# Kernel tuning notes

Hardware: AMD Instinct MI355X
Metric: run time of the kernel (lower is better)

The kernel has to match this reference:

```python
import jax, jax.numpy as jnp
import numpy as np

B, L, K, D = 32, 1024, 1024, 1024

def setup_inputs() -> dict:
    key = jax.random.key(0)
    k1, k2, k3, k4, k5 = jax.random.split(key, 5)
    query = jax.random.normal(k1, (B, L, D), dtype=jnp.float32)
    context = jax.random.normal(k2, (B, K, D), dtype=jnp.float32)
    mask = jax.random.randint(k3, (B * L, K), 0, 2, dtype=jnp.int32)
    W_in = jax.random.normal(k4, (D, D), dtype=jnp.float32) * (D ** -0.5)
    W_out = jax.random.normal(k5, (D, 2 * D), dtype=jnp.float32) * ((2 * D) ** -0.5)
    return {"query": query, "context": context, "mask": mask, "W_in": W_in, "W_out": W_out}

def reference(query, context, mask, W_in, W_out):
    b, l, d = query.shape
    k = context.shape[1]
    # linear_in (general attention): q @ W_in.T
    q = jnp.einsum('bld,ed->ble', query, W_in)
    # attention scores [b, l, k]
    scores = jnp.einsum('bld,bkd->blk', q, context)
    # multiplicative-mask softmax with renormalization (masked_softmax, non-memory-efficient path)
    m = mask.astype(scores.dtype).reshape(b, l, k)
    w = jax.nn.softmax(scores * m, axis=-1) * m
    w = w / (jnp.sum(w, axis=-1, keepdims=True) + 1e-13)
    # mix attended context, concat with transformed query, project, tanh
    mix = jnp.einsum('blk,bkd->bld', w, context)
    combined = jnp.concatenate([mix, q], axis=-1)          # [b, l, 2d]
    out = jnp.tanh(jnp.einsum('blc,dc->bld', combined, W_out))
    return out
```

## Files before the change

### kernel.cpp

```cpp
#include <hip/hip_runtime.h>
#include <math.h>

typedef __bf16 bf16_t;
typedef __bf16 bf16x4 __attribute__((ext_vector_type(4)));
typedef __bf16 bf16x8 __attribute__((ext_vector_type(8)));
typedef _Float16 f16x4 __attribute__((ext_vector_type(4)));
typedef _Float16 f16x8 __attribute__((ext_vector_type(8)));
typedef float f32x4 __attribute__((ext_vector_type(4)));

#define MFMA_BF16 __builtin_amdgcn_mfma_f32_16x16x32_bf16
#define MFMA_F16  __builtin_amdgcn_mfma_f32_16x16x32_f16


__device__ __forceinline__ bf16_t to_bf16_rne(float x, float& rep) {
    unsigned u = __builtin_bit_cast(unsigned, x);
    unsigned r = u + 0x7fffu + ((u >> 16) & 1u);
    unsigned short h = (unsigned short)(r >> 16);
    rep = __builtin_bit_cast(float, ((unsigned)h) << 16);
    return __builtin_bit_cast(bf16_t, h);
}

__device__ __forceinline__ void g2l16(const void* g, void* l) {
    __builtin_amdgcn_global_load_lds(
        (const __attribute__((address_space(1))) unsigned int*)g,
        (__attribute__((address_space(3))) unsigned int*)l, 16, 0, 0);
}

__device__ __forceinline__ int lch(int r, int j) {
    return (r * 8 + (j ^ (r & 7))) * 8;
}

template <typename T>
__device__ __forceinline__ void stage2(const T* __restrict__ gA, long long ldA,
                                       const T* __restrict__ gB, long long ldB,
                                       T* buf, int tid) {
    int wid = tid >> 6, lane = tid & 63;
#pragma unroll
    for (int i = 0; i < 4; ++i) {
        int cb = i * 512 + wid * 64;
        int c = cb + lane;
        int r = c >> 3, j = (c & 7) ^ (r & 7);
        g2l16(gA + (long long)r * ldA + j * 8, buf + (size_t)cb * 8);
    }
#pragma unroll
    for (int i = 0; i < 4; ++i) {
        int cb = i * 512 + wid * 64;
        int c = cb + lane;
        int r = c >> 3, j = (c & 7) ^ (r & 7);
        g2l16(gB + (long long)r * ldB + j * 8, buf + 16384 + (size_t)cb * 8);
    }
}


__global__ __launch_bounds__(256) void split_int_k(const float* __restrict__ in,
                                                   bf16_t* __restrict__ out,
                                                   long long n4) {
    long long i = (long long)blockIdx.x * 256 + threadIdx.x;
    if (i >= n4) return;
    f32x4 v = ((const f32x4*)in)[i];
    bf16x4 hv, lv;
#pragma unroll
    for (int j = 0; j < 4; ++j) {
        float rep;
        hv[j] = to_bf16_rne(v[j], rep);
        float res = v[j] - rep;
        float rep2;
        lv[j] = to_bf16_rne(res, rep2);
    }
    long long row = i >> 8;
    int k = (int)(i & 255) * 4;
    long long base = row * 2048 + ((k >> 5) << 6) + (k & 31);
    *(bf16x4*)(out + base) = hv;
    *(bf16x4*)(out + base + 32) = lv;
}

__global__ __launch_bounds__(256) void cast_f16_k(const float* __restrict__ in,
                                                  _Float16* __restrict__ o, long long n4) {
    long long i = (long long)blockIdx.x * 256 + threadIdx.x;
    if (i >= n4) return;
    f32x4 v = ((const f32x4*)in)[i];
    f16x4 h;
#pragma unroll
    for (int j = 0; j < 4; ++j) h[j] = (_Float16)v[j];
    ((f16x4*)o)[i] = h;
}

__global__ __launch_bounds__(256) void transpose_ctx_k(const float* __restrict__ ctx,
                                                       _Float16* __restrict__ ctxT) {
    __shared__ _Float16 t[32][34];
    int b = blockIdx.z;
    int k0 = blockIdx.x * 32, d0 = blockIdx.y * 32;
    const float* src = ctx + ((long long)b * 1024 + k0) * 1024 + d0;
#pragma unroll
    for (int i = 0; i < 4; ++i) {
        int y = threadIdx.y + i * 8;
        t[y][threadIdx.x] = (_Float16)src[(long long)y * 1024 + threadIdx.x];
    }
    __syncthreads();
    _Float16* dst = ctxT + ((long long)b * 1024 + d0) * 1024 + k0;
#pragma unroll
    for (int i = 0; i < 4; ++i) {
        int y = threadIdx.y + i * 8;
        dst[(long long)y * 1024 + threadIdx.x] = t[threadIdx.x][y];
    }
}

__global__ __launch_bounds__(256) void masked_softmax_k(const float* __restrict__ s,
                                                        const int* __restrict__ m,
                                                        _Float16* __restrict__ w) {
    long long row = blockIdx.x;
    const float* sr = s + row * 1024;
    const int* mr = m + row * 1024;
    _Float16* wr_ = w + row * 1024;
    int t = threadIdx.x;
    int lane = t & 63, wid = t >> 6;
    float v[4];
    int mk[4];
    float mx = -3.0e38f;
#pragma unroll
    for (int i = 0; i < 4; ++i) {
        int idx = t + i * 256;
        v[i] = sr[idx];
        mk[i] = mr[idx];
        if (mk[i]) mx = fmaxf(mx, v[i]);
    }
#pragma unroll
    for (int off = 32; off; off >>= 1) mx = fmaxf(mx, __shfl_xor(mx, off));
    __shared__ float rm[4], rs[4];
    if (!lane) rm[wid] = mx;
    __syncthreads();
    mx = fmaxf(fmaxf(rm[0], rm[1]), fmaxf(rm[2], rm[3]));
    float sum = 0.f;
#pragma unroll
    for (int i = 0; i < 4; ++i) {
        float e = mk[i] ? expf(v[i] - mx) : 0.f;
        v[i] = e;
        sum += e;
    }
#pragma unroll
    for (int off = 32; off; off >>= 1) sum += __shfl_xor(sum, off);
    if (!lane) rs[wid] = sum;
    __syncthreads();
    sum = rs[0] + rs[1] + rs[2] + rs[3];
    float inv = sum > 0.f ? 1.0f / sum : 0.f;
#pragma unroll
    for (int i = 0; i < 4; ++i) wr_[t + i * 256] = (_Float16)(v[i] * inv);
}

template <int EPI>
__global__ __launch_bounds__(512, 2) void gemm_x3_256(
    const bf16_t* __restrict__ Aint, const bf16_t* __restrict__ Bint,
    long long sA, long long sB, long long sC, int nbx, int nby,
    float* __restrict__ Cs, bf16_t* __restrict__ Qint, _Float16* __restrict__ Qf) {
    __shared__ bf16_t lds[65536];
    const int NT = 32;
    int tid = threadIdx.x, lane = tid & 63, wid = tid >> 6;
    int wr = wid >> 2, wc = wid & 3;
    int nwg = gridDim.x;
    int bid = blockIdx.x;
    int lid = (bid & 7) * (nwg >> 3) + (bid >> 3);
    int by = lid % nby;
    int t2 = lid / nby;
    int bx = t2 % nbx;
    int z = t2 / nbx;
    const bf16_t* At = Aint + (long long)z * sA + (long long)bx * 256 * 2048;
    const bf16_t* Bt = Bint + (long long)z * sB + (long long)by * 256 * 2048;
    stage2(At, 2048ll, Bt, 2048ll, lds, tid);
    stage2(At + 64, 2048ll, Bt + 64, 2048ll, lds + 32768, tid);
    f32x4 acc[8][4] = {};
    for (int t = 0; t < NT; ++t) {
        bf16_t* buf = lds + (size_t)(t & 1) * 32768;
        bf16_t* bufB = buf + 16384;
        if (t < NT - 1) {
            asm volatile("s_waitcnt vmcnt(8)" ::: "memory");
        } else {
            asm volatile("s_waitcnt vmcnt(0)" ::: "memory");
        }
        __builtin_amdgcn_sched_barrier(0);
        __builtin_amdgcn_s_barrier();
        __builtin_amdgcn_sched_barrier(0);
        bf16x8 bh[4], bl[4];
#pragma unroll
        for (int n = 0; n < 4; ++n) {
            int rB = wc * 64 + n * 16 + (lane & 15);
            bh[n] = *(const bf16x8*)(bufB + lch(rB, lane >> 4));
            bl[n] = *(const bf16x8*)(bufB + lch(rB, 4 + (lane >> 4)));
        }
#pragma unroll
        for (int p = 0; p < 3; ++p) {
            bf16x8 ah[2], al[2];
#pragma unroll
            for (int i = 0; i < 2; ++i) {
                int rA = wr * 128 + (p * 2 + i) * 16 + (lane & 15);
                ah[i] = *(const bf16x8*)(buf + lch(rA, lane >> 4));
                al[i] = *(const bf16x8*)(buf + lch(rA, 4 + (lane >> 4)));
            }
            __builtin_amdgcn_s_setprio(1);
#pragma unroll
            for (int i = 0; i < 2; ++i)
#pragma unroll
                for (int n = 0; n < 4; ++n) {
                    f32x4 a = acc[p * 2 + i][n];
                    a = MFMA_BF16(ah[i], bh[n], a, 0, 0, 0);
                    a = MFMA_BF16(ah[i], bl[n], a, 0, 0, 0);
                    a = MFMA_BF16(al[i], bh[n], a, 0, 0, 0);
                    acc[p * 2 + i][n] = a;
                }
            __builtin_amdgcn_s_setprio(0);
        }
        bf16x8 ah3[2], al3[2];
#pragma unroll
        for (int i = 0; i < 2; ++i) {
            int rA = wr * 128 + (6 + i) * 16 + (lane & 15);
            ah3[i] = *(const bf16x8*)(buf + lch(rA, lane >> 4));
            al3[i] = *(const bf16x8*)(buf + lch(rA, 4 + (lane >> 4)));
        }
        asm volatile("s_waitcnt lgkmcnt(0)" ::: "memory");
        __builtin_amdgcn_sched_barrier(0);
        __builtin_amdgcn_s_barrier();
        __builtin_amdgcn_sched_barrier(0);
        if (t + 2 < NT)
            stage2(At + (long long)(t + 2) * 64, 2048ll, Bt + (long long)(t + 2) * 64,
                   2048ll, buf, tid);
        __builtin_amdgcn_s_setprio(1);
#pragma unroll
        for (int i = 0; i < 2; ++i)
#pragma unroll
            for (int n = 0; n < 4; ++n) {
                f32x4 a = acc[6 + i][n];
                a = MFMA_BF16(ah3[i], bh[n], a, 0, 0, 0);
                a = MFMA_BF16(ah3[i], bl[n], a, 0, 0, 0);
                a = MFMA_BF16(al3[i], bh[n], a, 0, 0, 0);
                acc[6 + i][n] = a;
            }
        __builtin_amdgcn_s_setprio(0);
    }
    int r0 = bx * 256 + wr * 128 + ((lane >> 4) << 2);
    int c0 = by * 256 + wc * 64 + (lane & 15);
#pragma unroll
    for (int m = 0; m < 8; ++m)
#pragma unroll
        for (int n = 0; n < 4; ++n)
#pragma unroll
            for (int j = 0; j < 4; ++j) {
                int r = r0 + m * 16 + j;
                int c = c0 + n * 16;
                float v = acc[m][n][j];
                if (EPI == 0) {
                    Cs[(long long)z * sC + (long long)r * 1024 + c] = v;
                } else {
                    float rep;
                    bf16_t hb = to_bf16_rne(v, rep);
                    float res = v - rep;
                    float rep2;
                    bf16_t lb = to_bf16_rne(res, rep2);
                    long long rb = (long long)r * 2048 + ((c >> 5) << 6) + (c & 31);
                    Qint[rb] = hb;
                    Qint[rb + 32] = lb;
                    Qf[(long long)r * 1024 + c] = (_Float16)v;
                }
            }
}

template <int EPI>
__global__ __launch_bounds__(512, 2) void gemm_f16_256(
    const _Float16* __restrict__ A1, const _Float16* __restrict__ A2,
    const _Float16* __restrict__ B,
    long long ldA, long long ldB, long long sA, long long sB, long long sC,
    int NT, int swt, int nbx, int nby,
    _Float16* __restrict__ Cm, float* __restrict__ Co) {
    __shared__ _Float16 lds[65536];
    int tid = threadIdx.x, lane = tid & 63, wid = tid >> 6;
    int wr = wid >> 2, wc = wid & 3;
    int nwg = gridDim.x;
    int bid = blockIdx.x;
    int lid = (bid & 7) * (nwg >> 3) + (bid >> 3);
    int by = lid % nby;
    int t2 = lid / nby;
    int bx = t2 % nbx;
    int z = t2 / nbx;
    const _Float16* A1t = A1 + (long long)z * sA + (long long)bx * 256 * ldA;
    const _Float16* A2t = A2 + (long long)bx * 256 * ldA;
    const _Float16* Bt = B + (long long)z * sB + (long long)by * 256 * ldB;
    stage2((0 < swt) ? A1t : A2t, ldA, Bt, ldB, lds, tid);
    stage2((1 < swt) ? A1t + 64 : A2t + (long long)(1 - swt) * 64, ldA, Bt + 64, ldB,
           lds + 32768, tid);
    f32x4 acc[8][4] = {};
    for (int t = 0; t < NT; ++t) {
        _Float16* buf = lds + (size_t)(t & 1) * 32768;
        _Float16* bufB = buf + 16384;
        if (t < NT - 1) {
            asm volatile("s_waitcnt vmcnt(8)" ::: "memory");
        } else {
            asm volatile("s_waitcnt vmcnt(0)" ::: "memory");
        }
        __builtin_amdgcn_sched_barrier(0);
        __builtin_amdgcn_s_barrier();
        __builtin_amdgcn_sched_barrier(0);
        f16x8 bfr[4][2];
#pragma unroll
        for (int n = 0; n < 4; ++n)
#pragma unroll
            for (int ks = 0; ks < 2; ++ks) {
                int rB = wc * 64 + n * 16 + (lane & 15);
                bfr[n][ks] = *(const f16x8*)(bufB + lch(rB, ks * 4 + (lane >> 4)));
            }
#pragma unroll
        for (int p = 0; p < 3; ++p) {
            f16x8 a[2][2];
#pragma unroll
            for (int i = 0; i < 2; ++i)
#pragma unroll
                for (int ks = 0; ks < 2; ++ks) {
                    int rA = wr * 128 + (p * 2 + i) * 16 + (lane & 15);
                    a[i][ks] = *(const f16x8*)(buf + lch(rA, ks * 4 + (lane >> 4)));
                }
            __builtin_amdgcn_s_setprio(1);
#pragma unroll
            for (int i = 0; i < 2; ++i)
#pragma unroll
                for (int n = 0; n < 4; ++n) {
                    f32x4 v = acc[p * 2 + i][n];
                    v = MFMA_F16(a[i][0], bfr[n][0], v, 0, 0, 0);
                    v = MFMA_F16(a[i][1], bfr[n][1], v, 0, 0, 0);
                    acc[p * 2 + i][n] = v;
                }
            __builtin_amdgcn_s_setprio(0);
        }
        f16x8 a3[2][2];
#pragma unroll
        for (int i = 0; i < 2; ++i)
#pragma unroll
            for (int ks = 0; ks < 2; ++ks) {
                int rA = wr * 128 + (6 + i) * 16 + (lane & 15);
                a3[i][ks] = *(const f16x8*)(buf + lch(rA, ks * 4 + (lane >> 4)));
            }
        asm volatile("s_waitcnt lgkmcnt(0)" ::: "memory");
        __builtin_amdgcn_sched_barrier(0);
        __builtin_amdgcn_s_barrier();
        __builtin_amdgcn_sched_barrier(0);
        if (t + 2 < NT) {
            int tt = t + 2;
            const _Float16* gA =
                (tt < swt) ? A1t + (long long)tt * 64 : A2t + (long long)(tt - swt) * 64;
            stage2(gA, ldA, Bt + (long long)tt * 64, ldB, buf, tid);
        }
        __builtin_amdgcn_s_setprio(1);
#pragma unroll
        for (int i = 0; i < 2; ++i)
#pragma unroll
            for (int n = 0; n < 4; ++n) {
                f32x4 v = acc[6 + i][n];
                v = MFMA_F16(a3[i][0], bfr[n][0], v, 0, 0, 0);
                v = MFMA_F16(a3[i][1], bfr[n][1], v, 0, 0, 0);
                acc[6 + i][n] = v;
            }
        __builtin_amdgcn_s_setprio(0);
    }
    int r0 = bx * 256 + wr * 128 + ((lane >> 4) << 2);
    int c0 = by * 256 + wc * 64 + (lane & 15);
#pragma unroll
    for (int m = 0; m < 8; ++m)
#pragma unroll
        for (int n = 0; n < 4; ++n)
#pragma unroll
            for (int j = 0; j < 4; ++j) {
                int r = r0 + m * 16 + j;
                int c = c0 + n * 16;
                float v = acc[m][n][j];
                if (EPI == 0) {
                    Cm[(long long)z * sC + (long long)r * 1024 + c] = (_Float16)v;
                } else {
                    Co[(long long)r * 1024 + c] = tanhf(v);
                }
            }
}


extern "C" void kernel_launch(void* const* d_in, const int* in_sizes, int n_in,
                              void* d_out, int out_size, void* d_ws, size_t ws_size,
                              hipStream_t stream) {
    const float* query = (const float*)d_in[0];
    const float* ctx = (const float*)d_in[1];
    const int* mask = (const int*)d_in[2];
    const float* Win = (const float*)d_in[3];
    const float* Wout = (const float*)d_in[4];
    float* outp = (float*)d_out;

    const long long MB = 1048576ll;
    int G = 1;
    if ((long long)ws_size >= 648 * MB) G = 32;
    else if ((long long)ws_size >= 328 * MB) G = 16;
    else if ((long long)ws_size >= 168 * MB) G = 8;
    else if ((long long)ws_size >= 88 * MB) G = 4;
    else if ((long long)ws_size >= 48 * MB) G = 2;

    char* p = (char*)d_ws;
    bf16_t* win_int = (bf16_t*)p; p += 4 * MB;
    _Float16* woutf = (_Float16*)p; p += 4 * MB;
    const long long R = (long long)G * 1024;
    bf16_t* qint = (bf16_t*)p; p += 4 * G * MB;
    _Float16* qf = (_Float16*)p; p += 2 * G * MB;
    bf16_t* ctx_int = (bf16_t*)p; p += 4 * G * MB;
    _Float16* ctxT = (_Float16*)p; p += 2 * G * MB;
    _Float16* wf = (_Float16*)p; p += 2 * G * MB;
    _Float16* mixf = (_Float16*)p; p += 2 * G * MB;
    bf16_t* qs_int = (bf16_t*)p;
    float* scores = (float*)p;

    const long long LD = 1048576ll;

    split_int_k<<<1024, 256, 0, stream>>>(Win, win_int, 262144ll);
    cast_f16_k<<<2048, 256, 0, stream>>>(Wout, woutf, 524288ll);

    for (int b0 = 0; b0 < 32; b0 += G) {
        const float* qsrc = query + (long long)b0 * LD;
        const float* csrc = ctx + (long long)b0 * LD;
        split_int_k<<<(int)R, 256, 0, stream>>>(qsrc, qs_int, R * 256);
        gemm_x3_256<1><<<16 * G, 512, 0, stream>>>(
            qs_int, win_int, 0, 0, 0, 4 * G, 4, nullptr, qint, qf);
        split_int_k<<<(int)R, 256, 0, stream>>>(csrc, ctx_int, R * 256);
        transpose_ctx_k<<<dim3(32, 32, G), dim3(32, 8, 1), 0, stream>>>(csrc, ctxT);
        gemm_x3_256<0><<<16 * G, 512, 0, stream>>>(
            qint, ctx_int, 2097152ll, 2097152ll, 1048576ll, 4, 4,
            scores, nullptr, nullptr);
        masked_softmax_k<<<(int)R, 256, 0, stream>>>(
            scores, mask + (long long)b0 * 1024 * 1024, wf);
        gemm_f16_256<0><<<16 * G, 512, 0, stream>>>(
            wf, wf, ctxT, 1024ll, 1024ll, 1048576ll, 1048576ll, 1048576ll,
            16, 1 << 20, 4, 4, mixf, nullptr);
        gemm_f16_256<1><<<16 * G, 512, 0, stream>>>(
            mixf, qf, woutf, 1024ll, 2048ll, 0, 0, 0,
            32, 16, 4 * G, 4, nullptr, outp + (long long)b0 * LD);
    }
}
```

Before: 784.4 us.

## Shrink GEMM N-tile to 128 and switch to triple-buffered LDS pipeline

```diff
diff --git a/kernel.cpp b/kernel.cpp
--- a/kernel.cpp
+++ b/kernel.cpp
@@ -31,7 +31,7 @@
 }
 
 template <typename T>
-__device__ __forceinline__ void stage2(const T* __restrict__ gA, long long ldA,
+__device__ __forceinline__ void stage3(const T* __restrict__ gA, long long ldA,
                                        const T* __restrict__ gB, long long ldB,
                                        T* buf, int tid) {
     int wid = tid >> 6, lane = tid & 63;
@@ -43,7 +43,7 @@
         g2l16(gA + (long long)r * ldA + j * 8, buf + (size_t)cb * 8);
     }
 #pragma unroll
-    for (int i = 0; i < 4; ++i) {
+    for (int i = 0; i < 2; ++i) {
         int cb = i * 512 + wid * 64;
         int c = cb + lane;
         int r = c >> 3, j = (c & 7) ^ (r & 7);
@@ -148,11 +148,11 @@
 }
 
 template <int EPI>
-__global__ __launch_bounds__(512, 2) void gemm_x3_256(
+__global__ __launch_bounds__(512, 2) void gemm_x3_v2(
     const bf16_t* __restrict__ Aint, const bf16_t* __restrict__ Bint,
     long long sA, long long sB, long long sC, int nbx, int nby,
     float* __restrict__ Cs, bf16_t* __restrict__ Qint, _Float16* __restrict__ Qf) {
-    __shared__ bf16_t lds[65536];
+    __shared__ bf16_t lds[73728];
     const int NT = 32;
     int tid = threadIdx.x, lane = tid & 63, wid = tid >> 6;
     int wr = wid >> 2, wc = wid & 3;
@@ -164,83 +164,60 @@
     int bx = t2 % nbx;
     int z = t2 / nbx;
     const bf16_t* At = Aint + (long long)z * sA + (long long)bx * 256 * 2048;
-    const bf16_t* Bt = Bint + (long long)z * sB + (long long)by * 256 * 2048;
-    stage2(At, 2048ll, Bt, 2048ll, lds, tid);
-    stage2(At + 64, 2048ll, Bt + 64, 2048ll, lds + 32768, tid);
-    f32x4 acc[8][4] = {};
+    const bf16_t* Bt = Bint + (long long)z * sB + (long long)by * 128 * 2048;
+    stage3(At, 2048ll, Bt, 2048ll, lds, tid);
+    stage3(At + 64, 2048ll, Bt + 64, 2048ll, lds + 24576, tid);
+    f32x4 acc[8][2] = {};
     for (int t = 0; t < NT; ++t) {
-        bf16_t* buf = lds + (size_t)(t & 1) * 32768;
+        bf16_t* buf = lds + (size_t)(t % 3) * 24576;
         bf16_t* bufB = buf + 16384;
-        if (t < NT - 1) {
-            asm volatile("s_waitcnt vmcnt(8)" ::: "memory");
+        if (t + 1 < NT) {
+            asm volatile("s_waitcnt vmcnt(6)" ::: "memory");
         } else {
             asm volatile("s_waitcnt vmcnt(0)" ::: "memory");
         }
         __builtin_amdgcn_sched_barrier(0);
         __builtin_amdgcn_s_barrier();
         __builtin_amdgcn_sched_barrier(0);
-        bf16x8 bh[4], bl[4];
-#pragma unroll
-        for (int n = 0; n < 4; ++n) {
-            int rB = wc * 64 + n * 16 + (lane & 15);
+        if (t + 2 < NT)
+            stage3(At + (long long)(t + 2) * 64, 2048ll, Bt + (long long)(t + 2) * 64,
+                   2048ll, lds + (size_t)((t + 2) % 3) * 24576, tid);
+        bf16x8 bh[2], bl[2];
+#pragma unroll
+        for (int n = 0; n < 2; ++n) {
+            int rB = wc * 32 + n * 16 + (lane & 15);
             bh[n] = *(const bf16x8*)(bufB + lch(rB, lane >> 4));
             bl[n] = *(const bf16x8*)(bufB + lch(rB, 4 + (lane >> 4)));
         }
 #pragma unroll
-        for (int p = 0; p < 3; ++p) {
-            bf16x8 ah[2], al[2];
-#pragma unroll
-            for (int i = 0; i < 2; ++i) {
-                int rA = wr * 128 + (p * 2 + i) * 16 + (lane & 15);
+        for (int g = 0; g < 2; ++g) {
+            bf16x8 ah[4], al[4];
+#pragma unroll
+            for (int i = 0; i < 4; ++i) {
+                int rA = wr * 128 + (g * 4 + i) * 16 + (lane & 15);
                 ah[i] = *(const bf16x8*)(buf + lch(rA, lane >> 4));
                 al[i] = *(const bf16x8*)(buf + lch(rA, 4 + (lane >> 4)));
             }
             __builtin_amdgcn_s_setprio(1);
 #pragma unroll
-            for (int i = 0; i < 2; ++i)
-#pragma unroll
-                for (int n = 0; n < 4; ++n) {
-                    f32x4 a = acc[p * 2 + i][n];
+            for (int i = 0; i < 4; ++i)
+#pragma unroll
+                for (int n = 0; n < 2; ++n) {
+                    f32x4 a = acc[g * 4 + i][n];
                     a = MFMA_BF16(ah[i], bh[n], a, 0, 0, 0);
                     a = MFMA_BF16(ah[i], bl[n], a, 0, 0, 0);
                     a = MFMA_BF16(al[i], bh[n], a, 0, 0, 0);
-                    acc[p * 2 + i][n] = a;
+                    acc[g * 4 + i][n] = a;
                 }
             __builtin_amdgcn_s_setprio(0);
         }
-        bf16x8 ah3[2], al3[2];
-#pragma unroll
-        for (int i = 0; i < 2; ++i) {
-            int rA = wr * 128 + (6 + i) * 16 + (lane & 15);
-            ah3[i] = *(const bf16x8*)(buf + lch(rA, lane >> 4));
-            al3[i] = *(const bf16x8*)(buf + lch(rA, 4 + (lane >> 4)));
-        }
-        asm volatile("s_waitcnt lgkmcnt(0)" ::: "memory");
-        __builtin_amdgcn_sched_barrier(0);
-        __builtin_amdgcn_s_barrier();
-        __builtin_amdgcn_sched_barrier(0);
-        if (t + 2 < NT)
-            stage2(At + (long long)(t + 2) * 64, 2048ll, Bt + (long long)(t + 2) * 64,
-                   2048ll, buf, tid);
-        __builtin_amdgcn_s_setprio(1);
-#pragma unroll
-        for (int i = 0; i < 2; ++i)
-#pragma unroll
-            for (int n = 0; n < 4; ++n) {
-                f32x4 a = acc[6 + i][n];
-                a = MFMA_BF16(ah3[i], bh[n], a, 0, 0, 0);
-                a = MFMA_BF16(ah3[i], bl[n], a, 0, 0, 0);
-                a = MFMA_BF16(al3[i], bh[n], a, 0, 0, 0);
-                acc[6 + i][n] = a;
-            }
-        __builtin_amdgcn_s_setprio(0);
     }
     int r0 = bx * 256 + wr * 128 + ((lane >> 4) << 2);
-    int c0 = by * 256 + wc * 64 + (lane & 15);
+    int c0 = by * 128 + wc * 32 + (lane & 15);
 #pragma unroll
     for (int m = 0; m < 8; ++m)
 #pragma unroll
-        for (int n = 0; n < 4; ++n)
+        for (int n = 0; n < 2; ++n)
 #pragma unroll
             for (int j = 0; j < 4; ++j) {
                 int r = r0 + m * 16 + j;
@@ -263,13 +240,13 @@
 }
 
 template <int EPI>
-__global__ __launch_bounds__(512, 2) void gemm_f16_256(
+__global__ __launch_bounds__(512, 2) void gemm_f16_v2(
     const _Float16* __restrict__ A1, const _Float16* __restrict__ A2,
     const _Float16* __restrict__ B,
     long long ldA, long long ldB, long long sA, long long sB, long long sC,
     int NT, int swt, int nbx, int nby,
     _Float16* __restrict__ Cm, float* __restrict__ Co) {
-    __shared__ _Float16 lds[65536];
+    __shared__ _Float16 lds[73728];
     int tid = threadIdx.x, lane = tid & 63, wid = tid >> 6;
     int wr = wid >> 2, wc = wid & 3;
     int nwg = gridDim.x;
@@ -281,61 +258,19 @@
     int z = t2 / nbx;
     const _Float16* A1t = A1 + (long long)z * sA + (long long)bx * 256 * ldA;
     const _Float16* A2t = A2 + (long long)bx * 256 * ldA;
-    const _Float16* Bt = B + (long long)z * sB + (long long)by * 256 * ldB;
-    stage2((0 < swt) ? A1t : A2t, ldA, Bt, ldB, lds, tid);
-    stage2((1 < swt) ? A1t + 64 : A2t + (long long)(1 - swt) * 64, ldA, Bt + 64, ldB,
-           lds + 32768, tid);
-    f32x4 acc[8][4] = {};
+    const _Float16* Bt = B + (long long)z * sB + (long long)by * 128 * ldB;
+    stage3((0 < swt) ? A1t : A2t, ldA, Bt, ldB, lds, tid);
+    stage3((1 < swt) ? A1t + 64 : A2t + (long long)(1 - swt) * 64, ldA, Bt + 64, ldB,
+           lds + 24576, tid);
+    f32x4 acc[8][2] = {};
     for (int t = 0; t < NT; ++t) {
-        _Float16* buf = lds + (size_t)(t & 1) * 32768;
+        _Float16* buf = lds + (size_t)(t % 3) * 24576;
         _Float16* bufB = buf + 16384;
-        if (t < NT - 1) {
-            asm volatile("s_waitcnt vmcnt(8)" ::: "memory");
+        if (t + 1 < NT) {
+            asm volatile("s_waitcnt vmcnt(6)" ::: "memory");
         } else {
             asm volatile("s_waitcnt vmcnt(0)" ::: "memory");
         }
-        __builtin_amdgcn_sched_barrier(0);
-        __builtin_amdgcn_s_barrier();
-        __builtin_amdgcn_sched_barrier(0);
-        f16x8 bfr[4][2];
-#pragma unroll
-        for (int n = 0; n < 4; ++n)
-#pragma unroll
-            for (int ks = 0; ks < 2; ++ks) {
-                int rB = wc * 64 + n * 16 + (lane & 15);
-                bfr[n][ks] = *(const f16x8*)(bufB + lch(rB, ks * 4 + (lane >> 4)));
-            }
-#pragma unroll
-        for (int p = 0; p < 3; ++p) {
-            f16x8 a[2][2];
-#pragma unroll
-            for (int i = 0; i < 2; ++i)
-#pragma unroll
-                for (int ks = 0; ks < 2; ++ks) {
-                    int rA = wr * 128 + (p * 2 + i) * 16 + (lane & 15);
-                    a[i][ks] = *(const f16x8*)(buf + lch(rA, ks * 4 + (lane >> 4)));
-                }
-            __builtin_amdgcn_s_setprio(1);
-#pragma unroll
-            for (int i = 0; i < 2; ++i)
-#pragma unroll
-                for (int n = 0; n < 4; ++n) {
-                    f32x4 v = acc[p * 2 + i][n];
-                    v = MFMA_F16(a[i][0], bfr[n][0], v, 0, 0, 0);
-                    v = MFMA_F16(a[i][1], bfr[n][1], v, 0, 0, 0);
-                    acc[p * 2 + i][n] = v;
-                }
-            __builtin_amdgcn_s_setprio(0);
-        }
-        f16x8 a3[2][2];
-#pragma unroll
-        for (int i = 0; i < 2; ++i)
-#pragma unroll
-            for (int ks = 0; ks < 2; ++ks) {
-                int rA = wr * 128 + (6 + i) * 16 + (lane & 15);
-                a3[i][ks] = *(const f16x8*)(buf + lch(rA, ks * 4 + (lane >> 4)));
-            }
-        asm volatile("s_waitcnt lgkmcnt(0)" ::: "memory");
         __builtin_amdgcn_sched_barrier(0);
         __builtin_amdgcn_s_barrier();
         __builtin_amdgcn_sched_barrier(0);
@@ -343,26 +278,46 @@
             int tt = t + 2;
             const _Float16* gA =
                 (tt < swt) ? A1t + (long long)tt * 64 : A2t + (long long)(tt - swt) * 64;
-            stage2(gA, ldA, Bt + (long long)tt * 64, ldB, buf, tid);
-        }
-        __builtin_amdgcn_s_setprio(1);
-#pragma unroll
-        for (int i = 0; i < 2; ++i)
-#pragma unroll
-            for (int n = 0; n < 4; ++n) {
-                f32x4 v = acc[6 + i][n];
-                v = MFMA_F16(a3[i][0], bfr[n][0], v, 0, 0, 0);
-                v = MFMA_F16(a3[i][1], bfr[n][1], v, 0, 0, 0);
-                acc[6 + i][n] = v;
+            stage3(gA, ldA, Bt + (long long)tt * 64, ldB,
+                   lds + (size_t)(tt % 3) * 24576, tid);
+        }
+        f16x8 bfr[2][2];
+#pragma unroll
+        for (int n = 0; n < 2; ++n)
+#pragma unroll
+            for (int ks = 0; ks < 2; ++ks) {
+                int rB = wc * 32 + n * 16 + (lane & 15);
+                bfr[n][ks] = *(const f16x8*)(bufB + lch(rB, ks * 4 + (lane >> 4)));
             }
-        __builtin_amdgcn_s_setprio(0);
+#pragma unroll
+        for (int g = 0; g < 2; ++g) {
+            f16x8 a[4][2];
+#pragma unroll
+            for (int i = 0; i < 4; ++i)
+#pragma unroll
+                for (int ks = 0; ks < 2; ++ks) {
+                    int rA = wr * 128 + (g * 4 + i) * 16 + (lane & 15);
+                    a[i][ks] = *(const f16x8*)(buf + lch(rA, ks * 4 + (lane >> 4)));
+                }
+            __builtin_amdgcn_s_setprio(1);
+#pragma unroll
+            for (int i = 0; i < 4; ++i)
+#pragma unroll
+                for (int n = 0; n < 2; ++n) {
+                    f32x4 v = acc[g * 4 + i][n];
+                    v = MFMA_F16(a[i][0], bfr[n][0], v, 0, 0, 0);
+                    v = MFMA_F16(a[i][1], bfr[n][1], v, 0, 0, 0);
+                    acc[g * 4 + i][n] = v;
+                }
+            __builtin_amdgcn_s_setprio(0);
+        }
     }
     int r0 = bx * 256 + wr * 128 + ((lane >> 4) << 2);
-    int c0 = by * 256 + wc * 64 + (lane & 15);
+    int c0 = by * 128 + wc * 32 + (lane & 15);
 #pragma unroll
     for (int m = 0; m < 8; ++m)
 #pragma unroll
-        for (int n = 0; n < 4; ++n)
+        for (int n = 0; n < 2; ++n)
 #pragma unroll
             for (int j = 0; j < 4; ++j) {
                 int r = r0 + m * 16 + j;
@@ -417,20 +372,20 @@
         const float* qsrc = query + (long long)b0 * LD;
         const float* csrc = ctx + (long long)b0 * LD;
         split_int_k<<<(int)R, 256, 0, stream>>>(qsrc, qs_int, R * 256);
-        gemm_x3_256<1><<<16 * G, 512, 0, stream>>>(
-            qs_int, win_int, 0, 0, 0, 4 * G, 4, nullptr, qint, qf);
+        gemm_x3_v2<1><<<32 * G, 512, 0, stream>>>(
+            qs_int, win_int, 0, 0, 0, 4 * G, 8, nullptr, qint, qf);
         split_int_k<<<(int)R, 256, 0, stream>>>(csrc, ctx_int, R * 256);
         transpose_ctx_k<<<dim3(32, 32, G), dim3(32, 8, 1), 0, stream>>>(csrc, ctxT);
-        gemm_x3_256<0><<<16 * G, 512, 0, stream>>>(
-            qint, ctx_int, 2097152ll, 2097152ll, 1048576ll, 4, 4,
+        gemm_x3_v2<0><<<32 * G, 512, 0, stream>>>(
+            qint, ctx_int, 2097152ll, 2097152ll, 1048576ll, 4, 8,
             scores, nullptr, nullptr);
         masked_softmax_k<<<(int)R, 256, 0, stream>>>(
             scores, mask + (long long)b0 * 1024 * 1024, wf);
-        gemm_f16_256<0><<<16 * G, 512, 0, stream>>>(
+        gemm_f16_v2<0><<<32 * G, 512, 0, stream>>>(
             wf, wf, ctxT, 1024ll, 1024ll, 1048576ll, 1048576ll, 1048576ll,
-            16, 1 << 20, 4, 4, mixf, nullptr);
-        gemm_f16_256<1><<<16 * G, 512, 0, stream>>>(
+            16, 1 << 20, 4, 8, mixf, nullptr);
+        gemm_f16_v2<1><<<32 * G, 512, 0, stream>>>(
             mixf, qf, woutf, 1024ll, 2048ll, 0, 0, 0,
-            32, 16, 4 * G, 4, nullptr, outp + (long long)b0 * LD);
-    }
-}
+            32, 16, 4 * G, 8, nullptr, outp + (long long)b0 * LD);
+    }
+}
```

Measured after the change: 839.2 us. 1.07x slower.

## Switch GEMM kernels to 32x32x16 MFMA and alias workspace buffers

Applied to the files above, without the earlier changes.

```diff
diff --git a/kernel.cpp b/kernel.cpp
--- a/kernel.cpp
+++ b/kernel.cpp
@@ -7,9 +7,10 @@
 typedef _Float16 f16x4 __attribute__((ext_vector_type(4)));
 typedef _Float16 f16x8 __attribute__((ext_vector_type(8)));
 typedef float f32x4 __attribute__((ext_vector_type(4)));
-
-#define MFMA_BF16 __builtin_amdgcn_mfma_f32_16x16x32_bf16
-#define MFMA_F16  __builtin_amdgcn_mfma_f32_16x16x32_f16
+typedef float f32x16 __attribute__((ext_vector_type(16)));
+
+#define MFMA32B __builtin_amdgcn_mfma_f32_32x32x16_bf16
+#define MFMA32F __builtin_amdgcn_mfma_f32_32x32x16_f16
 
 
 __device__ __forceinline__ bf16_t to_bf16_rne(float x, float& rep) {
@@ -148,7 +149,7 @@
 }
 
 template <int EPI>
-__global__ __launch_bounds__(512, 2) void gemm_x3_256(
+__global__ __launch_bounds__(512, 2) void gemm_x3_w(
     const bf16_t* __restrict__ Aint, const bf16_t* __restrict__ Bint,
     long long sA, long long sB, long long sC, int nbx, int nby,
     float* __restrict__ Cs, bf16_t* __restrict__ Qint, _Float16* __restrict__ Qf) {
@@ -167,7 +168,8 @@
     const bf16_t* Bt = Bint + (long long)z * sB + (long long)by * 256 * 2048;
     stage2(At, 2048ll, Bt, 2048ll, lds, tid);
     stage2(At + 64, 2048ll, Bt + 64, 2048ll, lds + 32768, tid);
-    f32x4 acc[8][4] = {};
+    f32x16 acc[4][2] = {};
+    int l31 = lane & 31, lh = lane >> 5;
     for (int t = 0; t < NT; ++t) {
         bf16_t* buf = lds + (size_t)(t & 1) * 32768;
         bf16_t* bufB = buf + 16384;
@@ -179,41 +181,58 @@
         __builtin_amdgcn_sched_barrier(0);
         __builtin_amdgcn_s_barrier();
         __builtin_amdgcn_sched_barrier(0);
-        bf16x8 bh[4], bl[4];
-#pragma unroll
-        for (int n = 0; n < 4; ++n) {
-            int rB = wc * 64 + n * 16 + (lane & 15);
-            bh[n] = *(const bf16x8*)(bufB + lch(rB, lane >> 4));
-            bl[n] = *(const bf16x8*)(bufB + lch(rB, 4 + (lane >> 4)));
-        }
-#pragma unroll
-        for (int p = 0; p < 3; ++p) {
-            bf16x8 ah[2], al[2];
-#pragma unroll
-            for (int i = 0; i < 2; ++i) {
-                int rA = wr * 128 + (p * 2 + i) * 16 + (lane & 15);
-                ah[i] = *(const bf16x8*)(buf + lch(rA, lane >> 4));
-                al[i] = *(const bf16x8*)(buf + lch(rA, 4 + (lane >> 4)));
+        bf16x8 bh[2][2], bl[2][2];
+#pragma unroll
+        for (int n = 0; n < 2; ++n) {
+            int rB = wc * 64 + n * 32 + l31;
+#pragma unroll
+            for (int ks = 0; ks < 2; ++ks) {
+                bh[n][ks] = *(const bf16x8*)(bufB + lch(rB, ks * 2 + lh));
+                bl[n][ks] = *(const bf16x8*)(bufB + lch(rB, 4 + ks * 2 + lh));
             }
-            __builtin_amdgcn_s_setprio(1);
-#pragma unroll
-            for (int i = 0; i < 2; ++i)
-#pragma unroll
-                for (int n = 0; n < 4; ++n) {
-                    f32x4 a = acc[p * 2 + i][n];
-                    a = MFMA_BF16(ah[i], bh[n], a, 0, 0, 0);
-                    a = MFMA_BF16(ah[i], bl[n], a, 0, 0, 0);
-                    a = MFMA_BF16(al[i], bh[n], a, 0, 0, 0);
-                    acc[p * 2 + i][n] = a;
-                }
-            __builtin_amdgcn_s_setprio(0);
-        }
-        bf16x8 ah3[2], al3[2];
-#pragma unroll
-        for (int i = 0; i < 2; ++i) {
-            int rA = wr * 128 + (6 + i) * 16 + (lane & 15);
-            ah3[i] = *(const bf16x8*)(buf + lch(rA, lane >> 4));
-            al3[i] = *(const bf16x8*)(buf + lch(rA, 4 + (lane >> 4)));
+        }
+        bf16x8 ah[2][2], al[2][2];
+#pragma unroll
+        for (int mm = 0; mm < 2; ++mm) {
+            int rA = wr * 128 + mm * 32 + l31;
+#pragma unroll
+            for (int ks = 0; ks < 2; ++ks) {
+                ah[mm][ks] = *(const bf16x8*)(buf + lch(rA, ks * 2 + lh));
+                al[mm][ks] = *(const bf16x8*)(buf + lch(rA, 4 + ks * 2 + lh));
+            }
+        }
+        __builtin_amdgcn_s_setprio(1);
+#pragma unroll
+        for (int ks = 0; ks < 2; ++ks)
+#pragma unroll
+            for (int mm = 0; mm < 2; ++mm)
+#pragma unroll
+                for (int n = 0; n < 2; ++n)
+                    acc[mm][n] = MFMA32B(ah[mm][ks], bh[n][ks], acc[mm][n], 0, 0, 0);
+#pragma unroll
+        for (int ks = 0; ks < 2; ++ks)
+#pragma unroll
+            for (int mm = 0; mm < 2; ++mm)
+#pragma unroll
+                for (int n = 0; n < 2; ++n)
+                    acc[mm][n] = MFMA32B(ah[mm][ks], bl[n][ks], acc[mm][n], 0, 0, 0);
+#pragma unroll
+        for (int ks = 0; ks < 2; ++ks)
+#pragma unroll
+            for (int mm = 0; mm < 2; ++mm)
+#pragma unroll
+                for (int n = 0; n < 2; ++n)
+                    acc[mm][n] = MFMA32B(al[mm][ks], bh[n][ks], acc[mm][n], 0, 0, 0);
+        __builtin_amdgcn_s_setprio(0);
+        bf16x8 ah2[2][2], al2[2][2];
+#pragma unroll
+        for (int mm = 0; mm < 2; ++mm) {
+            int rA = wr * 128 + (2 + mm) * 32 + l31;
+#pragma unroll
+            for (int ks = 0; ks < 2; ++ks) {
+                ah2[mm][ks] = *(const bf16x8*)(buf + lch(rA, ks * 2 + lh));
+                al2[mm][ks] = *(const bf16x8*)(buf + lch(rA, 4 + ks * 2 + lh));
+            }
         }
         asm volatile("s_waitcnt lgkmcnt(0)" ::: "memory");
         __builtin_amdgcn_sched_barrier(0);
@@ -224,28 +243,39 @@
                    2048ll, buf, tid);
         __builtin_amdgcn_s_setprio(1);
 #pragma unroll
-        for (int i = 0; i < 2; ++i)
-#pragma unroll
-            for (int n = 0; n < 4; ++n) {
-                f32x4 a = acc[6 + i][n];
-                a = MFMA_BF16(ah3[i], bh[n], a, 0, 0, 0);
-                a = MFMA_BF16(ah3[i], bl[n], a, 0, 0, 0);
-                a = MFMA_BF16(al3[i], bh[n], a, 0, 0, 0);
-                acc[6 + i][n] = a;
-            }
+        for (int ks = 0; ks < 2; ++ks)
+#pragma unroll
+            for (int mm = 0; mm < 2; ++mm)
+#pragma unroll
+                for (int n = 0; n < 2; ++n)
+                    acc[2 + mm][n] = MFMA32B(ah2[mm][ks], bh[n][ks], acc[2 + mm][n], 0, 0, 0);
+#pragma unroll
+        for (int ks = 0; ks < 2; ++ks)
+#pragma unroll
+            for (int mm = 0; mm < 2; ++mm)
+#pragma unroll
+                for (int n = 0; n < 2; ++n)
+                    acc[2 + mm][n] = MFMA32B(ah2[mm][ks], bl[n][ks], acc[2 + mm][n], 0, 0, 0);
+#pragma unroll
+        for (int ks = 0; ks < 2; ++ks)
+#pragma unroll
+            for (int mm = 0; mm < 2; ++mm)
+#pragma unroll
+                for (int n = 0; n < 2; ++n)
+                    acc[2 + mm][n] = MFMA32B(al2[mm][ks], bh[n][ks], acc[2 + mm][n], 0, 0, 0);
         __builtin_amdgcn_s_setprio(0);
     }
-    int r0 = bx * 256 + wr * 128 + ((lane >> 4) << 2);
-    int c0 = by * 256 + wc * 64 + (lane & 15);
-#pragma unroll
-    for (int m = 0; m < 8; ++m)
-#pragma unroll
-        for (int n = 0; n < 4; ++n)
-#pragma unroll
-            for (int j = 0; j < 4; ++j) {
-                int r = r0 + m * 16 + j;
-                int c = c0 + n * 16;
-                float v = acc[m][n][j];
+    int r0 = bx * 256 + wr * 128 + 4 * lh;
+    int c0 = by * 256 + wc * 64 + l31;
+#pragma unroll
+    for (int m = 0; m < 4; ++m)
+#pragma unroll
+        for (int n = 0; n < 2; ++n)
+#pragma unroll
+            for (int reg = 0; reg < 16; ++reg) {
+                int r = r0 + m * 32 + (reg & 3) + 8 * (reg >> 2);
+                int c = c0 + n * 32;
+                float v = acc[m][n][reg];
                 if (EPI == 0) {
                     Cs[(long long)z * sC + (long long)r * 1024 + c] = v;
                 } else {
@@ -263,7 +293,7 @@
 }
 
 template <int EPI>
-__global__ __launch_bounds__(512, 2) void gemm_f16_256(
+__global__ __launch_bounds__(512, 2) void gemm_f16_w(
     const _Float16* __restrict__ A1, const _Float16* __restrict__ A2,
     const _Float16* __restrict__ B,
     long long ldA, long long ldB, long long sA, long long sB, long long sC,
@@ -285,7 +315,8 @@
     stage2((0 < swt) ? A1t : A2t, ldA, Bt, ldB, lds, tid);
     stage2((1 < swt) ? A1t + 64 : A2t + (long long)(1 - swt) * 64, ldA, Bt + 64, ldB,
            lds + 32768, tid);
-    f32x4 acc[8][4] = {};
+    f32x16 acc[4][2] = {};
+    int l31 = lane & 31, lh = lane >> 5;
     for (int t = 0; t < NT; ++t) {
         _Float16* buf = lds + (size_t)(t & 1) * 32768;
         _Float16* bufB = buf + 16384;
@@ -297,44 +328,39 @@
         __builtin_amdgcn_sched_barrier(0);
         __builtin_amdgcn_s_barrier();
         __builtin_amdgcn_sched_barrier(0);
-        f16x8 bfr[4][2];
-#pragma unroll
-        for (int n = 0; n < 4; ++n)
-#pragma unroll
-            for (int ks = 0; ks < 2; ++ks) {
-                int rB = wc * 64 + n * 16 + (lane & 15);
-                bfr[n][ks] = *(const f16x8*)(bufB + lch(rB, ks * 4 + (lane >> 4)));
-            }
-#pragma unroll
-        for (int p = 0; p < 3; ++p) {
-            f16x8 a[2][2];
-#pragma unroll
-            for (int i = 0; i < 2; ++i)
-#pragma unroll
-                for (int ks = 0; ks < 2; ++ks) {
-                    int rA = wr * 128 + (p * 2 + i) * 16 + (lane & 15);
-                    a[i][ks] = *(const f16x8*)(buf + lch(rA, ks * 4 + (lane >> 4)));
-                }
-            __builtin_amdgcn_s_setprio(1);
-#pragma unroll
-            for (int i = 0; i < 2; ++i)
-#pragma unroll
-                for (int n = 0; n < 4; ++n) {
-                    f32x4 v = acc[p * 2 + i][n];
-                    v = MFMA_F16(a[i][0], bfr[n][0], v, 0, 0, 0);
-                    v = MFMA_F16(a[i][1], bfr[n][1], v, 0, 0, 0);
-                    acc[p * 2 + i][n] = v;
-                }
-            __builtin_amdgcn_s_setprio(0);
-        }
-        f16x8 a3[2][2];
-#pragma unroll
-        for (int i = 0; i < 2; ++i)
-#pragma unroll
-            for (int ks = 0; ks < 2; ++ks) {
-                int rA = wr * 128 + (6 + i) * 16 + (lane & 15);
-                a3[i][ks] = *(const f16x8*)(buf + lch(rA, ks * 4 + (lane >> 4)));
-            }
+        f16x8 bfr[2][4];
+#pragma unroll
+        for (int n = 0; n < 2; ++n) {
+            int rB = wc * 64 + n * 32 + l31;
+#pragma unroll
+            for (int ks = 0; ks < 4; ++ks)
+                bfr[n][ks] = *(const f16x8*)(bufB + lch(rB, ks * 2 + lh));
+        }
+        f16x8 a[2][4];
+#pragma unroll
+        for (int mm = 0; mm < 2; ++mm) {
+            int rA = wr * 128 + mm * 32 + l31;
+#pragma unroll
+            for (int ks = 0; ks < 4; ++ks)
+                a[mm][ks] = *(const f16x8*)(buf + lch(rA, ks * 2 + lh));
+        }
+        __builtin_amdgcn_s_setprio(1);
+#pragma unroll
+        for (int ks = 0; ks < 4; ++ks)
+#pragma unroll
+            for (int mm = 0; mm < 2; ++mm)
+#pragma unroll
+                for (int n = 0; n < 2; ++n)
+                    acc[mm][n] = MFMA32F(a[mm][ks], bfr[n][ks], acc[mm][n], 0, 0, 0);
+        __builtin_amdgcn_s_setprio(0);
+        f16x8 a2[2][4];
+#pragma unroll
+        for (int mm = 0; mm < 2; ++mm) {
+            int rA = wr * 128 + (2 + mm) * 32 + l31;
+#pragma unroll
+            for (int ks = 0; ks < 4; ++ks)
+                a2[mm][ks] = *(const f16x8*)(buf + lch(rA, ks * 2 + lh));
+        }
         asm volatile("s_waitcnt lgkmcnt(0)" ::: "memory");
         __builtin_amdgcn_sched_barrier(0);
         __builtin_amdgcn_s_barrier();
@@ -343,31 +369,30 @@
             int tt = t + 2;
             const _Float16* gA =
                 (tt < swt) ? A1t + (long long)tt * 64 : A2t + (long long)(tt - swt) * 64;
-            stage2(gA, ldA, Bt + (long long)tt * 64, ldB, buf, tid);
+            stage2(gA, ldA, Bt + (long long)tt * 64, ldB,
+                   lds + (size_t)(tt & 1) * 32768, tid);
         }
         __builtin_amdgcn_s_setprio(1);
 #pragma unroll
-        for (int i = 0; i < 2; ++i)
-#pragma unroll
-            for (int n = 0; n < 4; ++n) {
-                f32x4 v = acc[6 + i][n];
-                v = MFMA_F16(a3[i][0], bfr[n][0], v, 0, 0, 0);
-                v = MFMA_F16(a3[i][1], bfr[n][1], v, 0, 0, 0);
-                acc[6 + i][n] = v;
-            }
+        for (int ks = 0; ks < 4; ++ks)
+#pragma unroll
+            for (int mm = 0; mm < 2; ++mm)
+#pragma unroll
+                for (int n = 0; n < 2; ++n)
+                    acc[2 + mm][n] = MFMA32F(a2[mm][ks], bfr[n][ks], acc[2 + mm][n], 0, 0, 0);
         __builtin_amdgcn_s_setprio(0);
     }
-    int r0 = bx * 256 + wr * 128 + ((lane >> 4) << 2);
-    int c0 = by * 256 + wc * 64 + (lane & 15);
-#pragma unroll
-    for (int m = 0; m < 8; ++m)
-#pragma unroll
-        for (int n = 0; n < 4; ++n)
-#pragma unroll
-            for (int j = 0; j < 4; ++j) {
-                int r = r0 + m * 16 + j;
-                int c = c0 + n * 16;
-                float v = acc[m][n][j];
+    int r0 = bx * 256 + wr * 128 + 4 * lh;
+    int c0 = by * 256 + wc * 64 + l31;
+#pragma unroll
+    for (int m = 0; m < 4; ++m)
+#pragma unroll
+        for (int n = 0; n < 2; ++n)
+#pragma unroll
+            for (int reg = 0; reg < 16; ++reg) {
+                int r = r0 + m * 32 + (reg & 3) + 8 * (reg >> 2);
+                int c = c0 + n * 32;
+                float v = acc[m][n][reg];
                 if (EPI == 0) {
                     Cm[(long long)z * sC + (long long)r * 1024 + c] = (_Float16)v;
                 } else {
@@ -389,11 +414,11 @@
 
     const long long MB = 1048576ll;
     int G = 1;
-    if ((long long)ws_size >= 648 * MB) G = 32;
-    else if ((long long)ws_size >= 328 * MB) G = 16;
-    else if ((long long)ws_size >= 168 * MB) G = 8;
-    else if ((long long)ws_size >= 88 * MB) G = 4;
-    else if ((long long)ws_size >= 48 * MB) G = 2;
+    if ((long long)ws_size >= 520 * MB) G = 32;
+    else if ((long long)ws_size >= 264 * MB) G = 16;
+    else if ((long long)ws_size >= 136 * MB) G = 8;
+    else if ((long long)ws_size >= 72 * MB) G = 4;
+    else if ((long long)ws_size >= 40 * MB) G = 2;
 
     char* p = (char*)d_ws;
     bf16_t* win_int = (bf16_t*)p; p += 4 * MB;
@@ -401,12 +426,14 @@
     const long long R = (long long)G * 1024;
     bf16_t* qint = (bf16_t*)p; p += 4 * G * MB;
     _Float16* qf = (_Float16*)p; p += 2 * G * MB;
-    bf16_t* ctx_int = (bf16_t*)p; p += 4 * G * MB;
+    char* slabA = p; p += 4 * G * MB;
+    bf16_t* ctx_int = (bf16_t*)slabA;
+    _Float16* wf = (_Float16*)slabA;
+    _Float16* mixf = (_Float16*)(slabA + 2 * G * MB);
     _Float16* ctxT = (_Float16*)p; p += 2 * G * MB;
-    _Float16* wf = (_Float16*)p; p += 2 * G * MB;
-    _Float16* mixf = (_Float16*)p; p += 2 * G * MB;
-    bf16_t* qs_int = (bf16_t*)p;
-    float* scores = (float*)p;
+    char* slabC = p;
+    bf16_t* qs_int = (bf16_t*)slabC;
+    float* scores = (float*)slabC;
 
     const long long LD = 1048576ll;
 
@@ -417,19 +444,19 @@
         const float* qsrc = query + (long long)b0 * LD;
         const float* csrc = ctx + (long long)b0 * LD;
         split_int_k<<<(int)R, 256, 0, stream>>>(qsrc, qs_int, R * 256);
-        gemm_x3_256<1><<<16 * G, 512, 0, stream>>>(
+        gemm_x3_w<1><<<16 * G, 512, 0, stream>>>(
             qs_int, win_int, 0, 0, 0, 4 * G, 4, nullptr, qint, qf);
         split_int_k<<<(int)R, 256, 0, stream>>>(csrc, ctx_int, R * 256);
         transpose_ctx_k<<<dim3(32, 32, G), dim3(32, 8, 1), 0, stream>>>(csrc, ctxT);
-        gemm_x3_256<0><<<16 * G, 512, 0, stream>>>(
+        gemm_x3_w<0><<<16 * G, 512, 0, stream>>>(
             qint, ctx_int, 2097152ll, 2097152ll, 1048576ll, 4, 4,
             scores, nullptr, nullptr);
         masked_softmax_k<<<(int)R, 256, 0, stream>>>(
             scores, mask + (long long)b0 * 1024 * 1024, wf);
-        gemm_f16_256<0><<<16 * G, 512, 0, stream>>>(
+        gemm_f16_w<0><<<16 * G, 512, 0, stream>>>(
             wf, wf, ctxT, 1024ll, 1024ll, 1048576ll, 1048576ll, 1048576ll,
             16, 1 << 20, 4, 4, mixf, nullptr);
-        gemm_f16_256<1><<<16 * G, 512, 0, stream>>>(
+        gemm_f16_w<1><<<16 * G, 512, 0, stream>>>(
             mixf, qf, woutf, 1024ll, 2048ll, 0, 0, 0,
             32, 16, 4 * G, 4, nullptr, outp + (long long)b0 * LD);
     }
```

After: 831.0 us. 1.06x slower.
